# Kernel tuning notes

Measured on AMD Instinct MI355X. Metric: run time of the kernel, lower is better.

Reference implementation:

```python
import jax, jax.numpy as jnp
import numpy as np
from jax import lax

B, C, TX, TY = 16, 192, 512, 2048
SEG = 8192 // 256  # segment_frames = 32 (hop length 256)
NEG_INF = -1e9


def setup_inputs() -> dict:
    key = jax.random.key(0)
    ks = jax.random.split(key, 7)
    z = jax.random.normal(ks[0], (B, C, TY), jnp.float32)
    z_p = jax.random.normal(ks[1], (B, C, TY), jnp.float32)
    m_p = jax.random.normal(ks[2], (B, C, TX), jnp.float32)
    logs_p = 0.1 * jax.random.normal(ks[3], (B, C, TX), jnp.float32)
    x_lengths = jax.random.randint(ks[4], (B,), TX // 2, TX + 1, jnp.int32)
    y_lengths = jax.random.randint(ks[5], (B,), TY // 2, TY + 1, jnp.int32)
    rand_u = jax.random.uniform(ks[6], (B,), jnp.float32)
    return dict(z=z, z_p=z_p, m_p=m_p, logs_p=logs_p,
                x_lengths=x_lengths, y_lengths=y_lengths, rand_u=rand_u)


def neg_cent_fn(z_p, m_p, logs_p):
    # sum_c -0.5 * exp(-2 logs)[c,tx] * (z_p[c,ty] - m_p[c,tx])^2 - sum_c logs[c,tx]
    # expanded (z-m)^2 = z^2 - 2 z m + m^2 -> batched GEMMs (same math as broadcast form)
    s = jnp.exp(-2.0 * logs_p)                                 # [B,C,Tx]
    a = jnp.einsum('bct,bcs->bts', -0.5 * z_p * z_p, s)        # [B,Ty,Tx]
    b = jnp.einsum('bct,bcs->bts', z_p, s * m_p)               # [B,Ty,Tx]
    c = jnp.sum(-0.5 * s * m_p * m_p - logs_p, axis=1)         # [B,Tx]
    return a + b + c[:, None, :]


def maximum_path_single(value, t_x, t_y):
    # Monotonic alignment search DP on value [Ty,Tx], valid region [:t_y,:t_x].
    Ty, Tx = value.shape
    tx = jnp.arange(Tx)

    def fwd(v, row):
        v_shift = jnp.concatenate([jnp.full((1,), NEG_INF, v.dtype), v[:-1]])
        dirn = v_shift > v                      # True: best predecessor is tx-1
        v_new = row + jnp.maximum(v, v_shift)
        v_new = jnp.where(tx < t_x, v_new, NEG_INF)
        v_new = jnp.maximum(v_new, NEG_INF)     # clamp accumulation
        return v_new, dirn

    v0 = jnp.where(tx == 0, 0.0, NEG_INF)
    _, dirs = lax.scan(fwd, v0, value)          # dirs [Ty,Tx] bool

    def bwd(idx, j):
        active = j < t_y
        idx = jnp.where(j == t_y - 1, t_x - 1, idx)
        row = jnp.where(active, jnp.zeros((Tx,), value.dtype).at[idx].set(1.0), 0.0)
        idx = jnp.where(active, idx - dirs[j, idx].astype(idx.dtype), idx)
        return idx, row

    _, path_rev = lax.scan(bwd, jnp.int32(0), jnp.arange(Ty - 1, -1, -1))
    return path_rev[::-1]                       # [Ty,Tx] 0/1 path


def rand_slice_segments(z, y_lengths, rand_u):
    t = z.shape[2]
    safe = jnp.minimum(y_lengths, t)
    ids_max = jnp.maximum(safe - SEG, 0)
    ids = (rand_u * (ids_max.astype(jnp.float32) + 1e-8)).astype(jnp.int32)
    zs = jax.vmap(lambda zi, s: lax.dynamic_slice_in_dim(zi, s, SEG, axis=1))(z, ids)
    valid = (jnp.arange(SEG)[None, None, :] < (safe - ids)[:, None, None])
    return zs * valid.astype(z.dtype), ids


def reference(z, z_p, m_p, logs_p, x_lengths, y_lengths, rand_u):
    neg_cent = neg_cent_fn(z_p, m_p, logs_p)                     # [B,Ty,Tx]
    attn = jax.vmap(maximum_path_single)(neg_cent, x_lengths, y_lengths)
    attn = lax.stop_gradient(attn)                               # torch: no_grad + detach
    m_p_a = jnp.einsum('bts,bcs->bct', attn, m_p)                # [B,C,Ty]
    logs_p_a = jnp.einsum('bts,bcs->bct', attn, logs_p)          # [B,C,Ty]
    z_slice, ids_slice = rand_slice_segments(z, y_lengths, rand_u)
    return z_slice, ids_slice, attn, m_p_a, logs_p_a
```

## Files before the change

### kernel.cpp

```cpp
#include <hip/hip_runtime.h>
#include <stdint.h>

#define B_   16
#define C_   192
#define TX_  512
#define TY_  2048
#define K_   384
#define SEG_ 32
#define NEG_INF_ (-1e9f)


__global__ __launch_bounds__(128) void k_prep(const float* __restrict__ mp,
                                              const float* __restrict__ logsp,
                                              float* __restrict__ Bmat,
                                              float* __restrict__ cterm) {
    int b  = blockIdx.y;
    int tx = blockIdx.x * 128 + threadIdx.x;
    const float* mb = mp    + (size_t)b * C_ * TX_ + tx;
    const float* lb = logsp + (size_t)b * C_ * TX_ + tx;
    float* B0 = Bmat + (size_t)b * K_ * TX_ + tx;
    float acc = 0.f;
    for (int c = 0; c < C_; ++c) {
        float lg = lb[(size_t)c * TX_];
        float m  = mb[(size_t)c * TX_];
        float s  = expf(-2.f * lg);
        B0[(size_t)c * TX_]        = s;
        B0[(size_t)(C_ + c) * TX_] = s * m;
        acc += -0.5f * s * m * m - lg;
    }
    cterm[b * TX_ + tx] = acc;
}

__global__ __launch_bounds__(256) void k_gemm(const float* __restrict__ zp,
                                              const float* __restrict__ Bmat,
                                              const float* __restrict__ cterm,
                                              float* __restrict__ ncout) {
    __shared__ float As[16][128];
    __shared__ float Bs[16][128];
    int b  = blockIdx.z;
    int m0 = blockIdx.y * 128;
    int n0 = blockIdx.x * 128;
    int tid = threadIdx.x;
    int tm = tid >> 4;
    int tn = tid & 15;
    const float* zpb = zp   + (size_t)b * C_ * TY_;
    const float* Bb  = Bmat + (size_t)b * K_ * TX_;

    float acc[8][8];
#pragma unroll
    for (int i = 0; i < 8; ++i)
#pragma unroll
        for (int j = 0; j < 8; ++j) acc[i][j] = 0.f;

    int lrow = tid >> 5;
    int lcol = (tid & 31) << 2;

    for (int k0 = 0; k0 < K_; k0 += 16) {
        int ksrc = (k0 < C_) ? k0 : (k0 - C_);
        const float* Ab = zpb + (size_t)(ksrc + lrow) * TY_ + m0 + lcol;
        float4 z0 = *(const float4*)Ab;
        float4 z1 = *(const float4*)(Ab + (size_t)8 * TY_);
        if (k0 < C_) {
            z0.x = -0.5f * z0.x * z0.x; z0.y = -0.5f * z0.y * z0.y;
            z0.z = -0.5f * z0.z * z0.z; z0.w = -0.5f * z0.w * z0.w;
            z1.x = -0.5f * z1.x * z1.x; z1.y = -0.5f * z1.y * z1.y;
            z1.z = -0.5f * z1.z * z1.z; z1.w = -0.5f * z1.w * z1.w;
        }
        const float* Bp = Bb + (size_t)(k0 + lrow) * TX_ + n0 + lcol;
        float4 w0 = *(const float4*)Bp;
        float4 w1 = *(const float4*)(Bp + (size_t)8 * TX_);

        __syncthreads();
        *(float4*)&As[lrow][lcol]     = z0;
        *(float4*)&As[lrow + 8][lcol] = z1;
        *(float4*)&Bs[lrow][lcol]     = w0;
        *(float4*)&Bs[lrow + 8][lcol] = w1;
        __syncthreads();

#pragma unroll
        for (int kk = 0; kk < 16; ++kk) {
            float4 a0 = *(const float4*)&As[kk][tm * 8];
            float4 a1 = *(const float4*)&As[kk][tm * 8 + 4];
            float4 b0 = *(const float4*)&Bs[kk][tn * 8];
            float4 b1 = *(const float4*)&Bs[kk][tn * 8 + 4];
            float a[8]  = {a0.x, a0.y, a0.z, a0.w, a1.x, a1.y, a1.z, a1.w};
            float bb[8] = {b0.x, b0.y, b0.z, b0.w, b1.x, b1.y, b1.z, b1.w};
#pragma unroll
            for (int i = 0; i < 8; ++i)
#pragma unroll
                for (int j = 0; j < 8; ++j)
                    acc[i][j] = fmaf(a[i], bb[j], acc[i][j]);
        }
    }

    float cadd[8];
#pragma unroll
    for (int j = 0; j < 8; ++j) cadd[j] = cterm[b * TX_ + n0 + tn * 8 + j];

#pragma unroll
    for (int i = 0; i < 8; ++i) {
        int row = m0 + tm * 8 + i;
        float* orow = ncout + ((size_t)b * TY_ + row) * TX_ + n0 + tn * 8;
        float4 o0, o1;
        o0.x = acc[i][0] + cadd[0]; o0.y = acc[i][1] + cadd[1];
        o0.z = acc[i][2] + cadd[2]; o0.w = acc[i][3] + cadd[3];
        o1.x = acc[i][4] + cadd[4]; o1.y = acc[i][5] + cadd[5];
        o1.z = acc[i][6] + cadd[6]; o1.w = acc[i][7] + cadd[7];
        *(float4*)orow       = o0;
        *(float4*)(orow + 4) = o1;
    }
}

#define LOADG(g, P0, P1)                                                     \
    {                                                                        \
        const float* rp = base + (size_t)(g) * 8 * TX_;                      \
        _Pragma("unroll") for (int r = 0; r < 8; ++r) {                      \
            P0[r] = *(const float4*)(rp + (size_t)r * TX_);                  \
            P1[r] = *(const float4*)(rp + (size_t)r * TX_ + 4);              \
        }                                                                    \
    }

#define PROCG(g, P0, P1)                                                     \
    {                                                                        \
        unsigned dw0 = 0u, dw1 = 0u;                                         \
        _Pragma("unroll") for (int r = 0; r < 8; ++r) {                      \
            float rc[8] = {P0[r].x, P0[r].y, P0[r].z, P0[r].w,               \
                           P1[r].x, P1[r].y, P1[r].z, P1[r].w};              \
            float left = __shfl_up(v[7], 1);                                 \
            if (lane == 0) left = NEG_INF_;                                  \
            unsigned by = 0u;                                                \
            _Pragma("unroll") for (int k = 7; k >= 0; --k) {                 \
                float vs = (k == 0) ? left : v[k - 1];                       \
                if (vs > v[k]) by |= (1u << k);                              \
                v[k] = fmaxf(v[k], vs) + rc[k];                              \
            }                                                                \
            if (r < 4) dw0 |= by << (8 * r);                                 \
            else       dw1 |= by << (8 * (r - 4));                           \
        }                                                                    \
        sdirs32[((g) * 2) * 64 + lane]     = dw0;                            \
        sdirs32[((g) * 2 + 1) * 64 + lane] = dw1;                            \
    }

__global__ __launch_bounds__(64, 1) void k_dp(const float* __restrict__ nc,
                                              const int* __restrict__ xl,
                                              const int* __restrict__ yl,
                                              int* __restrict__ path) {
    extern __shared__ unsigned char sdirs[];
    unsigned* sdirs32 = (unsigned*)sdirs;
    int b    = blockIdx.x;
    int lane = threadIdx.x;
    int t_x  = xl[b];
    int t_y  = yl[b]; if (t_y > TY_) t_y = TY_;
    const float* base = nc + (size_t)b * TY_ * TX_ + lane * 8;

    int col0 = lane * 8;
    float v[8];
#pragma unroll
    for (int k = 0; k < 8; ++k) v[k] = (col0 + k == 0) ? 0.f : NEG_INF_;

    float4 c0[8], c1[8], n0[8], n1[8];
    int ng = (t_y + 7) >> 3;

    LOADG(0, c0, c1);
    for (int g = 0; g < ng; g += 2) {
        if (g + 1 < ng) LOADG(g + 1, n0, n1);
        __builtin_amdgcn_sched_barrier(0);
        PROCG(g, c0, c1);
        if (g + 1 < ng) {
            if (g + 2 < ng) LOADG(g + 2, c0, c1);
            __builtin_amdgcn_sched_barrier(0);
            PROCG(g + 1, n0, n1);
        }
    }

    __syncthreads();

    int* pb = path + b * TY_;
    for (int j = t_y + lane; j < TY_; j += 64) pb[j] = -1;

    if (lane == 0) {
        int idx = t_x - 1;
        int j   = t_y - 1;
        while (j >= 0) {
            int n  = (j + 1 < 8) ? (j + 1) : 8;
            int bs = (idx - 7) >> 3; if (bs < 0) bs = 0;
            int b2 = bs + 1;         if (b2 > 63) b2 = 63;
            unsigned lo[8], hi[8];
#pragma unroll
            for (int r = 0; r < 8; ++r) {
                if (r < n) {
                    int jr = j - r;
                    int rb = (jr >> 2) * 256 + (jr & 3);
                    lo[r] = sdirs[rb + bs * 4];
                    hi[r] = sdirs[rb + b2 * 4];
                }
            }
#pragma unroll
            for (int r = 0; r < 8; ++r) {
                if (r < n) {
                    pb[j - r] = idx;
                    int Bi = idx >> 3;
                    unsigned byte = (Bi == bs) ? lo[r] : hi[r];
                    idx -= (int)((byte >> (idx & 7)) & 1u);
                }
            }
            j -= n;
        }
    }
}

__global__ __launch_bounds__(256) void k_attn(const int* __restrict__ path,
                                              float* __restrict__ attn) {
    int i   = blockIdx.x * 256 + threadIdx.x;
    int tx0 = (i & 127) << 2;
    int bty = i >> 7;
    int p   = path[bty];
    float4 o;
    o.x = (p == tx0)     ? 1.f : 0.f;
    o.y = (p == tx0 + 1) ? 1.f : 0.f;
    o.z = (p == tx0 + 2) ? 1.f : 0.f;
    o.w = (p == tx0 + 3) ? 1.f : 0.f;
    ((float4*)attn)[i] = o;
}

__global__ __launch_bounds__(256) void k_proj(const int* __restrict__ path,
                                              const float* __restrict__ mp,
                                              const float* __restrict__ logsp,
                                              float* __restrict__ mpa,
                                              float* __restrict__ logsa) {
    int i   = blockIdx.x * 256 + threadIdx.x;
    int ty0 = (i & 511) << 2;
    int bc  = i >> 9;
    int b   = bc / C_;
    const int4 p4 = *(const int4*)(path + b * TY_ + ty0);
    const float* mrow = mp    + (size_t)bc * TX_;
    const float* lrow = logsp + (size_t)bc * TX_;
    float4 mo, lo;
    mo.x = (p4.x >= 0) ? mrow[p4.x] : 0.f;  lo.x = (p4.x >= 0) ? lrow[p4.x] : 0.f;
    mo.y = (p4.y >= 0) ? mrow[p4.y] : 0.f;  lo.y = (p4.y >= 0) ? lrow[p4.y] : 0.f;
    mo.z = (p4.z >= 0) ? mrow[p4.z] : 0.f;  lo.z = (p4.z >= 0) ? lrow[p4.z] : 0.f;
    mo.w = (p4.w >= 0) ? mrow[p4.w] : 0.f;  lo.w = (p4.w >= 0) ? lrow[p4.w] : 0.f;
    ((float4*)mpa)[i]   = mo;
    ((float4*)logsa)[i] = lo;
}

__global__ __launch_bounds__(256) void k_slice(const float* __restrict__ z,
                                               const int* __restrict__ yl,
                                               const float* __restrict__ ru,
                                               float* __restrict__ zs,
                                               float* __restrict__ oid) {
    int b = blockIdx.x;
    int safe = yl[b]; if (safe > TY_) safe = TY_;
    int idsmax = safe - SEG_; if (idsmax < 0) idsmax = 0;
    int ids = (int)(ru[b] * ((float)idsmax + 1e-8f));
    int lim = safe - ids;
    for (int t = threadIdx.x; t < C_ * SEG_; t += 256) {
        int c = t >> 5, k = t & 31;
        zs[b * C_ * SEG_ + t] =
            (k < lim) ? z[((size_t)b * C_ + c) * TY_ + ids + k] : 0.f;
    }
    if (threadIdx.x == 0) oid[b] = (float)ids;
}

extern "C" void kernel_launch(void* const* d_in, const int* in_sizes, int n_in,
                              void* d_out, int out_size, void* d_ws, size_t ws_size,
                              hipStream_t stream) {
    const float* z     = (const float*)d_in[0];
    const float* zp    = (const float*)d_in[1];
    const float* mp    = (const float*)d_in[2];
    const float* logsp = (const float*)d_in[3];
    const int*   xl    = (const int*)d_in[4];
    const int*   yl    = (const int*)d_in[5];
    const float* ru    = (const float*)d_in[6];

    float* out     = (float*)d_out;
    float* o_zs    = out;
    float* o_ids   = out + 98304;
    float* o_attn  = out + 98320;
    float* o_mpa   = out + 16875536;
    float* o_logsa = out + 23166992;

    float* Bmat  = (float*)d_ws;
    float* cterm = Bmat + (size_t)B_ * K_ * TX_;
    int*   path  = (int*)(cterm + B_ * TX_);

    hipFuncSetAttribute((const void*)k_dp,
                        hipFuncAttributeMaxDynamicSharedMemorySize,
                        TY_ * 64);

    hipLaunchKernelGGL(k_prep, dim3(TX_ / 128, B_), dim3(128), 0, stream,
                       mp, logsp, Bmat, cterm);
    hipLaunchKernelGGL(k_gemm, dim3(TX_ / 128, TY_ / 128, B_), dim3(256), 0, stream,
                       zp, Bmat, cterm, o_attn);
    hipLaunchKernelGGL(k_dp, dim3(B_), dim3(64), TY_ * 64, stream,
                       o_attn, xl, yl, path);
    hipLaunchKernelGGL(k_attn, dim3(B_ * TY_ * TX_ / 4 / 256), dim3(256), 0, stream,
                       path, o_attn);
    hipLaunchKernelGGL(k_proj, dim3(B_ * C_ * TY_ / 4 / 256), dim3(256), 0, stream,
                       path, mp, logsp, o_mpa, o_logsa);
    hipLaunchKernelGGL(k_slice, dim3(B_), dim3(256), 0, stream,
                       z, yl, ru, o_zs, o_ids);
}
```

Measured before the change: 772.6 us.

## Stream DP rows through LDS with async global_load_lds triple buffering

Replaces the register double-buffered prefetch of neg_cent rows in the DP kernel with asynchronous global-to-LDS loads into a three-deep ring of 4-row stages, waiting on vmcnt before each stage is processed. The aim is to keep more memory requests in flight and relieve register pressure in the latency-bound single-wave sequential scan. The cost is extra LDS (24 KB), LDS read traffic, explicit waitcnt handling, and a smaller 4-row group that stores direction bits in one dword per group.

```diff
diff --git a/kernel.cpp b/kernel.cpp
--- a/kernel.cpp
+++ b/kernel.cpp
@@ -111,21 +111,38 @@
     }
 }
 
-#define LOADG(g, P0, P1)                                                     \
+typedef const uint32_t __attribute__((address_space(1)))* gas1_t;
+typedef uint32_t       __attribute__((address_space(3)))* las3_t;
+#define GLOADLDS(gp, lp)                                                     \
+    __builtin_amdgcn_global_load_lds((gas1_t)(const void*)(gp),              \
+                                     (las3_t)(void*)(lp), 16, 0, 0)
+
+#define ISSUEG(gg, buf)                                                      \
     {                                                                        \
-        const float* rp = base + (size_t)(g) * 8 * TX_;                      \
-        _Pragma("unroll") for (int r = 0; r < 8; ++r) {                      \
-            P0[r] = *(const float4*)(rp + (size_t)r * TX_);                  \
-            P1[r] = *(const float4*)(rp + (size_t)r * TX_ + 4);              \
+        int gsrc = ((gg) < ng) ? (gg) : (ng - 1);                            \
+        const float* gp = ncb + (size_t)gsrc * 4 * TX_;                      \
+        float* lb = stage + (buf) * 2048;                                    \
+        _Pragma("unroll") for (int r = 0; r < 4; ++r) {                      \
+            GLOADLDS(gp + (size_t)r * TX_ + lane * 8,     lb + r * 512);     \
+            GLOADLDS(gp + (size_t)r * TX_ + lane * 8 + 4, lb + r * 512 + 256);\
         }                                                                    \
     }
 
-#define PROCG(g, P0, P1)                                                     \
+#define WAITG                                                                \
+    do {                                                                     \
+        asm volatile("s_waitcnt vmcnt(16)" ::: "memory");                    \
+        __builtin_amdgcn_sched_barrier(0);                                   \
+    } while (0)
+
+#define PROCG(g, buf)                                                        \
     {                                                                        \
-        unsigned dw0 = 0u, dw1 = 0u;                                         \
-        _Pragma("unroll") for (int r = 0; r < 8; ++r) {                      \
-            float rc[8] = {P0[r].x, P0[r].y, P0[r].z, P0[r].w,               \
-                           P1[r].x, P1[r].y, P1[r].z, P1[r].w};              \
+        const float* lb = stage + (buf) * 2048 + lane * 4;                   \
+        unsigned dw0 = 0u;                                                   \
+        _Pragma("unroll") for (int r = 0; r < 4; ++r) {                      \
+            float4 q0 = *(const float4*)(lb + r * 512);                      \
+            float4 q1 = *(const float4*)(lb + r * 512 + 256);                \
+            float rc[8] = {q0.x, q0.y, q0.z, q0.w,                           \
+                           q1.x, q1.y, q1.z, q1.w};                          \
             float left = __shfl_up(v[7], 1);                                 \
             if (lane == 0) left = NEG_INF_;                                  \
             unsigned by = 0u;                                                \
@@ -134,11 +151,9 @@
                 if (vs > v[k]) by |= (1u << k);                              \
                 v[k] = fmaxf(v[k], vs) + rc[k];                              \
             }                                                                \
-            if (r < 4) dw0 |= by << (8 * r);                                 \
-            else       dw1 |= by << (8 * (r - 4));                           \
+            dw0 |= by << (8 * r);                                            \
         }                                                                    \
-        sdirs32[((g) * 2) * 64 + lane]     = dw0;                            \
-        sdirs32[((g) * 2 + 1) * 64 + lane] = dw1;                            \
+        sdirs32[(g) * 64 + lane] = dw0;                                      \
     }
 
 __global__ __launch_bounds__(64, 1) void k_dp(const float* __restrict__ nc,
@@ -147,31 +162,34 @@
                                               int* __restrict__ path) {
     extern __shared__ unsigned char sdirs[];
     unsigned* sdirs32 = (unsigned*)sdirs;
+    float*    stage   = (float*)(sdirs + TY_ * 64);
     int b    = blockIdx.x;
     int lane = threadIdx.x;
     int t_x  = xl[b];
     int t_y  = yl[b]; if (t_y > TY_) t_y = TY_;
-    const float* base = nc + (size_t)b * TY_ * TX_ + lane * 8;
+    const float* ncb = nc + (size_t)b * TY_ * TX_;
 
     int col0 = lane * 8;
     float v[8];
 #pragma unroll
     for (int k = 0; k < 8; ++k) v[k] = (col0 + k == 0) ? 0.f : NEG_INF_;
 
-    float4 c0[8], c1[8], n0[8], n1[8];
-    int ng = (t_y + 7) >> 3;
-
-    LOADG(0, c0, c1);
-    for (int g = 0; g < ng; g += 2) {
-        if (g + 1 < ng) LOADG(g + 1, n0, n1);
+    int ng = (t_y + 3) >> 2;
+
+    ISSUEG(0, 0);
+    ISSUEG(1, 1);
+    ISSUEG(2, 2);
+    int buf = 0;
+    for (int g = 0; g < ng; ++g) {
+        WAITG;
+        PROCG(g, buf);
+        asm volatile("s_waitcnt lgkmcnt(0)" ::: "memory");
         __builtin_amdgcn_sched_barrier(0);
-        PROCG(g, c0, c1);
-        if (g + 1 < ng) {
-            if (g + 2 < ng) LOADG(g + 2, c0, c1);
-            __builtin_amdgcn_sched_barrier(0);
-            PROCG(g + 1, n0, n1);
-        }
-    }
+        ISSUEG(g + 3, buf);
+        buf = (buf == 2) ? 0 : buf + 1;
+    }
+    asm volatile("s_waitcnt vmcnt(0)" ::: "memory");
+    __builtin_amdgcn_sched_barrier(0);
 
     __syncthreads();
 
@@ -286,13 +304,13 @@
 
     hipFuncSetAttribute((const void*)k_dp,
                         hipFuncAttributeMaxDynamicSharedMemorySize,
-                        TY_ * 64);
+                        TY_ * 64 + 24576);
 
     hipLaunchKernelGGL(k_prep, dim3(TX_ / 128, B_), dim3(128), 0, stream,
                        mp, logsp, Bmat, cterm);
     hipLaunchKernelGGL(k_gemm, dim3(TX_ / 128, TY_ / 128, B_), dim3(256), 0, stream,
                        zp, Bmat, cterm, o_attn);
-    hipLaunchKernelGGL(k_dp, dim3(B_), dim3(64), TY_ * 64, stream,
+    hipLaunchKernelGGL(k_dp, dim3(B_), dim3(64), TY_ * 64 + 24576, stream,
                        o_attn, xl, yl, path);
     hipLaunchKernelGGL(k_attn, dim3(B_ * TY_ * TX_ / 4 / 256), dim3(256), 0, stream,
                        path, o_attn);
```

After: 876.6 us. +13.5%, slower.

## Warp-specialize DP kernel with producer waves staging rows through LDS ring

Applied to the files above, without the earlier changes.

The single-wave DP kernel, which loaded neg_cent rows from global memory itself, becomes a block of nine waves. Eight producer waves prefetch 8-row groups into an 8-slot LDS ring, and one consumer wave runs the recurrence, signalling through volatile flags. Direction bits now go to a global scratch area (the m_p_a output buffer) and are copied back into LDS before the backtrack, because the staging ring reuses that shared memory. The aim is to hide global load latency on the serial critical path. In exchange it adds spin-wait synchronization with timeout fallbacks and an extra global round trip for the direction bits.

```diff
diff --git a/kernel.cpp b/kernel.cpp
--- a/kernel.cpp
+++ b/kernel.cpp
@@ -8,6 +8,9 @@
 #define K_   384
 #define SEG_ 32
 #define NEG_INF_ (-1e9f)
+
+#define NPROD_ 8
+#define NSLOT_ 8
 
 
 __global__ __launch_bounds__(128) void k_prep(const float* __restrict__ mp,
@@ -111,74 +114,120 @@
     }
 }
 
-#define LOADG(g, P0, P1)                                                     \
-    {                                                                        \
-        const float* rp = base + (size_t)(g) * 8 * TX_;                      \
-        _Pragma("unroll") for (int r = 0; r < 8; ++r) {                      \
-            P0[r] = *(const float4*)(rp + (size_t)r * TX_);                  \
-            P1[r] = *(const float4*)(rp + (size_t)r * TX_ + 4);              \
-        }                                                                    \
-    }
-
-#define PROCG(g, P0, P1)                                                     \
-    {                                                                        \
-        unsigned dw0 = 0u, dw1 = 0u;                                         \
-        _Pragma("unroll") for (int r = 0; r < 8; ++r) {                      \
-            float rc[8] = {P0[r].x, P0[r].y, P0[r].z, P0[r].w,               \
-                           P1[r].x, P1[r].y, P1[r].z, P1[r].w};              \
-            float left = __shfl_up(v[7], 1);                                 \
-            if (lane == 0) left = NEG_INF_;                                  \
-            unsigned by = 0u;                                                \
-            _Pragma("unroll") for (int k = 7; k >= 0; --k) {                 \
-                float vs = (k == 0) ? left : v[k - 1];                       \
-                if (vs > v[k]) by |= (1u << k);                              \
-                v[k] = fmaxf(v[k], vs) + rc[k];                              \
-            }                                                                \
-            if (r < 4) dw0 |= by << (8 * r);                                 \
-            else       dw1 |= by << (8 * (r - 4));                           \
-        }                                                                    \
-        sdirs32[((g) * 2) * 64 + lane]     = dw0;                            \
-        sdirs32[((g) * 2 + 1) * 64 + lane] = dw1;                            \
-    }
-
-__global__ __launch_bounds__(64, 1) void k_dp(const float* __restrict__ nc,
-                                              const int* __restrict__ xl,
-                                              const int* __restrict__ yl,
-                                              int* __restrict__ path) {
+__global__ __launch_bounds__(576, 1) void k_dp(const float* __restrict__ nc,
+                                               const int* __restrict__ xl,
+                                               const int* __restrict__ yl,
+                                               int* __restrict__ path,
+                                               int* __restrict__ gdirs) {
     extern __shared__ unsigned char sdirs[];
     unsigned* sdirs32 = (unsigned*)sdirs;
+    float*    stage   = (float*)sdirs;
+    volatile int* vpf = (volatile int*)(sdirs + 131072);
+    volatile int* vcf = (volatile int*)(sdirs + 131072 + 64);
     int b    = blockIdx.x;
-    int lane = threadIdx.x;
+    int tid  = threadIdx.x;
+    int wid  = tid >> 6;
+    int lane = tid & 63;
     int t_x  = xl[b];
     int t_y  = yl[b]; if (t_y > TY_) t_y = TY_;
-    const float* base = nc + (size_t)b * TY_ * TX_ + lane * 8;
-
-    int col0 = lane * 8;
-    float v[8];
-#pragma unroll
-    for (int k = 0; k < 8; ++k) v[k] = (col0 + k == 0) ? 0.f : NEG_INF_;
-
-    float4 c0[8], c1[8], n0[8], n1[8];
+    const float* ncb = nc + (size_t)b * TY_ * TX_;
+    int* gd32 = gdirs + b * (TY_ * 64 / 4);
+
     int ng = (t_y + 7) >> 3;
 
-    LOADG(0, c0, c1);
-    for (int g = 0; g < ng; g += 2) {
-        if (g + 1 < ng) LOADG(g + 1, n0, n1);
-        __builtin_amdgcn_sched_barrier(0);
-        PROCG(g, c0, c1);
-        if (g + 1 < ng) {
-            if (g + 2 < ng) LOADG(g + 2, c0, c1);
+    if (tid < NSLOT_) vpf[tid] = -1;
+    if (tid == NSLOT_) vcf[0] = -1;
+    __syncthreads();
+
+    if (wid == 0) {
+        int col0 = lane * 8;
+        float v[8];
+#pragma unroll
+        for (int k = 0; k < 8; ++k) v[k] = (col0 + k == 0) ? 0.f : NEG_INF_;
+
+        for (int g = 0; g < ng; ++g) {
+            int slot = g & (NSLOT_ - 1);
+            int spin = 0;
+            bool lds_ok = true;
+            while (vpf[slot] != g) {
+                if (++spin > 512) { lds_ok = false; break; }
+            }
             __builtin_amdgcn_sched_barrier(0);
-            PROCG(g + 1, n0, n1);
+            const float* lb = stage + slot * 4096 + lane * 4;
+            const float* gp = ncb + (size_t)g * 8 * TX_ + lane * 8;
+            unsigned dw0 = 0u, dw1 = 0u;
+#pragma unroll
+            for (int r = 0; r < 8; ++r) {
+                float4 q0, q1;
+                if (lds_ok) {
+                    q0 = *(const float4*)(lb + r * 512);
+                    q1 = *(const float4*)(lb + r * 512 + 256);
+                } else {
+                    q0 = *(const float4*)(gp + (size_t)r * TX_);
+                    q1 = *(const float4*)(gp + (size_t)r * TX_ + 4);
+                }
+                float rc[8] = {q0.x, q0.y, q0.z, q0.w,
+                               q1.x, q1.y, q1.z, q1.w};
+                float left = __shfl_up(v[7], 1);
+                if (lane == 0) left = NEG_INF_;
+                unsigned by = 0u;
+#pragma unroll
+                for (int k = 7; k >= 0; --k) {
+                    float vs = (k == 0) ? left : v[k - 1];
+                    if (vs > v[k]) by |= (1u << k);
+                    v[k] = fmaxf(v[k], vs) + rc[k];
+                }
+                if (r < 4) dw0 |= by << (8 * r);
+                else       dw1 |= by << (8 * (r - 4));
+            }
+            gd32[(2 * g)     * 64 + lane] = (int)dw0;
+            gd32[(2 * g + 1) * 64 + lane] = (int)dw1;
+            __builtin_amdgcn_sched_barrier(0);
+            __threadfence_block();
+            if (lane == 0) vcf[0] = g;
+        }
+    } else {
+        int w = wid - 1;
+        float* lb = stage + w * 4096 + lane * 4;
+        bool alive = true;
+        for (int g = w; alive && g < ng; g += NPROD_) {
+            int spin = 0;
+            while (vcf[0] < g - NSLOT_) {
+                __builtin_amdgcn_s_sleep(2);
+                if (++spin > (1 << 14)) { alive = false; break; }
+            }
+            if (!alive) break;
+            __builtin_amdgcn_sched_barrier(0);
+            const float* gp = ncb + (size_t)g * 8 * TX_ + lane * 8;
+            float4 q[8], p[8];
+#pragma unroll
+            for (int r = 0; r < 8; ++r) {
+                q[r] = *(const float4*)(gp + (size_t)r * TX_);
+                p[r] = *(const float4*)(gp + (size_t)r * TX_ + 4);
+            }
+#pragma unroll
+            for (int r = 0; r < 8; ++r) {
+                *(float4*)(lb + r * 512)       = q[r];
+                *(float4*)(lb + r * 512 + 256) = p[r];
+            }
+            __threadfence_block();
+            if (lane == 0) vpf[w] = g;
         }
     }
 
     __syncthreads();
 
+    {
+        const float4* g4 = (const float4*)gd32;
+        float4* s4 = (float4*)sdirs;
+        for (int i = tid; i < TY_ * 16 / 4; i += 576) s4[i] = g4[i];
+    }
+    __syncthreads();
+
     int* pb = path + b * TY_;
-    for (int j = t_y + lane; j < TY_; j += 64) pb[j] = -1;
-
-    if (lane == 0) {
+    for (int j = t_y + tid; j < TY_; j += 576) pb[j] = -1;
+
+    if (tid == 0) {
         int idx = t_x - 1;
         int j   = t_y - 1;
         while (j >= 0) {
@@ -283,17 +332,18 @@
     float* Bmat  = (float*)d_ws;
     float* cterm = Bmat + (size_t)B_ * K_ * TX_;
     int*   path  = (int*)(cterm + B_ * TX_);
+    int*   gdirs = (int*)o_mpa;
 
     hipFuncSetAttribute((const void*)k_dp,
                         hipFuncAttributeMaxDynamicSharedMemorySize,
-                        TY_ * 64);
+                        TY_ * 64 + 256);
 
     hipLaunchKernelGGL(k_prep, dim3(TX_ / 128, B_), dim3(128), 0, stream,
                        mp, logsp, Bmat, cterm);
     hipLaunchKernelGGL(k_gemm, dim3(TX_ / 128, TY_ / 128, B_), dim3(256), 0, stream,
                        zp, Bmat, cterm, o_attn);
-    hipLaunchKernelGGL(k_dp, dim3(B_), dim3(64), TY_ * 64, stream,
-                       o_attn, xl, yl, path);
+    hipLaunchKernelGGL(k_dp, dim3(B_), dim3(576), TY_ * 64 + 256, stream,
+                       o_attn, xl, yl, path, gdirs);
     hipLaunchKernelGGL(k_attn, dim3(B_ * TY_ * TX_ / 4 / 256), dim3(256), 0, stream,
                        path, o_attn);
     hipLaunchKernelGGL(k_proj, dim3(B_ * C_ * TY_ / 4 / 256), dim3(256), 0, stream,
```

Result: slower. 936.4 us (+21.2%).
